# Kernel optimization log

Measured on AMD Instinct MI355X. Metric: run time of the kernel, lower is better.

Reference implementation:

```python
import jax, jax.numpy as jnp
import numpy as np

N, DIM, H, W = 8, 64, 256, 256
K = 3            # strip kernel size
EPS = 1e-5       # BatchNorm eps


def setup_inputs() -> dict:
    key = jax.random.key(0)
    kx, kh, kw = jax.random.split(key, 3)
    x = jax.random.normal(kx, (N, DIM, H, W), jnp.float32)

    def branch_params(k):
        k1, k2, k3, k4, k5 = jax.random.split(k, 5)
        w = jax.random.normal(k1, (DIM * K, DIM), jnp.float32) / np.sqrt(DIM).astype(np.float32)
        g = jax.random.uniform(k2, (DIM * K,), jnp.float32, 0.5, 1.5)   # BN weight
        b = jax.random.normal(k3, (DIM * K,), jnp.float32) * 0.1       # BN bias
        m = jax.random.normal(k4, (DIM * K,), jnp.float32) * 0.1       # BN running_mean
        v = jax.random.uniform(k5, (DIM * K,), jnp.float32, 0.5, 1.5)  # BN running_var
        return w, g, b, m, v

    wH, gH, bH, mH, vH = branch_params(kh)
    wW, gW, bW, mW, vW = branch_params(kw)
    return dict(x=x, wH=wH, gH=gH, bH=bH, mH=mH, vH=vH,
                wW=wW, gW=gW, bW=bW, mW=mW, vW=vW)


def _strip_att(x, w, g, b, m, v, horizontal):
    # Dynamic per-sample, per-channel 1D strip filter (involution-style).
    n, c, h, wd = x.shape
    gap = x.mean(axis=(2, 3))                       # (n, c)  AdaptiveAvgPool2d(1,1)
    f = gap @ w.T                                   # (n, c*K) 1x1 conv, no bias
    f = (f - m) * (g / jnp.sqrt(v + EPS)) + b       # BatchNorm2d (eval mode)
    f = jnp.tanh(f).reshape(n, c, K)                # per-(sample,channel) kernel taps
    pad = (K - 1) // 2
    if horizontal:  # kernel (1, K), reflect-pad width
        xp = jnp.pad(x, ((0, 0), (0, 0), (0, 0), (pad, pad)), mode='reflect')
        win = jnp.stack([xp[..., j:j + wd] for j in range(K)], axis=-1)  # (n,c,h,w,K)
    else:           # kernel (K, 1), reflect-pad height
        xp = jnp.pad(x, ((0, 0), (0, 0), (pad, pad), (0, 0)), mode='reflect')
        win = jnp.stack([xp[:, :, j:j + h, :] for j in range(K)], axis=-1)
    # grouped conv with groups = n*dim == depthwise correlation with dynamic taps
    return jnp.einsum('nchwk,nck->nchw', win, f)


def reference(x, wH, gH, bH, mH, vH, wW, gW, bW, mW, vW):
    out1 = _strip_att(x, wH, gH, bH, mH, vH, True)   # H_spatial_att (1,K) kernel
    out2 = _strip_att(x, wW, gW, bW, mW, vW, False)  # W_spatial_att (K,1) kernel
    return jnp.concatenate((out1, out2), axis=1)     # (n, 2c, h, w)
```

## Files before the change

kernel.cpp:

```cpp
#include <hip/hip_runtime.h>
#include <math.h>

#define N 8
#define DIM 64
#define H 256
#define W 256
#define K 3
#define EPS 1e-5f
#define TH 32

__global__ void gap_kernel(const float* __restrict__ x, float* __restrict__ gap) {
    const int plane = blockIdx.x;
    const float4* p4 = (const float4*)(x + (size_t)plane * (H * W));
    const int tid = threadIdx.x;
    float s = 0.f;
    #pragma unroll 4
    for (int i = tid; i < (H * W) / 4; i += 256) {
        float4 v = p4[i];
        s += (v.x + v.y) + (v.z + v.w);
    }
    __shared__ float red[256];
    red[tid] = s;
    __syncthreads();
    for (int off = 128; off > 0; off >>= 1) {
        if (tid < off) red[tid] += red[tid + off];
        __syncthreads();
    }
    if (tid == 0) gap[plane] = red[0] * (1.0f / (H * W));
}

__global__ void taps_kernel(const float* __restrict__ gap,
                            const float* __restrict__ wH, const float* __restrict__ gH,
                            const float* __restrict__ bH, const float* __restrict__ mH,
                            const float* __restrict__ vH,
                            const float* __restrict__ wW, const float* __restrict__ gW,
                            const float* __restrict__ bW, const float* __restrict__ mW,
                            const float* __restrict__ vW,
                            float* __restrict__ taps) {
    int idx = blockIdx.x * blockDim.x + threadIdx.x;
    if (idx >= 2 * N * DIM * K) return;
    const int branch = idx / (N * DIM * K);
    const int rem    = idx % (N * DIM * K);
    const int n      = rem / (DIM * K);
    const int j      = rem % (DIM * K);
    const float* w = branch ? wW : wH;
    const float* g = branch ? gW : gH;
    const float* b = branch ? bW : bH;
    const float* m = branch ? mW : mH;
    const float* v = branch ? vW : vH;
    const float* grow = gap + n * DIM;
    const float* wrow = w + (size_t)j * DIM;
    float acc = 0.f;
    #pragma unroll
    for (int d = 0; d < DIM; d++) acc += grow[d] * wrow[d];
    float f = (acc - m[j]) * (g[j] * rsqrtf(v[j] + EPS)) + b[j];
    taps[idx] = tanhf(f);
}

__global__ __launch_bounds__(256) void conv_kernel(const float* __restrict__ x,
                                                   const float* __restrict__ taps,
                                                   float* __restrict__ out) {
    __shared__ float tile[TH + 2][W];
    const int plane = blockIdx.y;
    const int n = plane / DIM;
    const int c = plane % DIM;
    const int h0 = blockIdx.x * TH;
    const int w = threadIdx.x;

    const float* xp = x + (size_t)plane * (H * W);

    #pragma unroll
    for (int r = 0; r < TH + 2; r++) {
        int hh = h0 - 1 + r;
        if (hh < 0) hh = -hh;
        if (hh >= H) hh = 2 * H - 2 - hh;
        tile[r][w] = xp[hh * W + w];
    }
    __syncthreads();

    const float* tH = taps + (n * DIM + c) * K;
    const float* tW = taps + N * DIM * K + (n * DIM + c) * K;
    const float tH0 = tH[0], tH1 = tH[1], tH2 = tH[2];
    const float tW0 = tW[0], tW1 = tW[1], tW2 = tW[2];

    float* out1 = out + (((size_t)n * 2 * DIM + c) * H + h0) * W;
    float* out2 = out + (((size_t)n * 2 * DIM + DIM + c) * H + h0) * W;

    const int wm = (w == 0) ? 1 : w - 1;
    const int wp = (w == W - 1) ? W - 2 : w + 1;

    #pragma unroll 4
    for (int r = 0; r < TH; r++) {
        const float xc = tile[r + 1][w];
        const float o1 = tile[r + 1][wm] * tH0 + xc * tH1 + tile[r + 1][wp] * tH2;
        const float o2 = tile[r][w] * tW0 + xc * tW1 + tile[r + 2][w] * tW2;
        out1[r * W + w] = o1;
        out2[r * W + w] = o2;
    }
}

extern "C" void kernel_launch(void* const* d_in, const int* in_sizes, int n_in,
                              void* d_out, int out_size, void* d_ws, size_t ws_size,
                              hipStream_t stream) {
    const float* x  = (const float*)d_in[0];
    const float* wH = (const float*)d_in[1];
    const float* gH = (const float*)d_in[2];
    const float* bH = (const float*)d_in[3];
    const float* mH = (const float*)d_in[4];
    const float* vH = (const float*)d_in[5];
    const float* wW = (const float*)d_in[6];
    const float* gW = (const float*)d_in[7];
    const float* bW = (const float*)d_in[8];
    const float* mW = (const float*)d_in[9];
    const float* vW = (const float*)d_in[10];
    float* out = (float*)d_out;

    float* gap  = (float*)d_ws;
    float* taps = gap + N * DIM;

    gap_kernel<<<N * DIM, 256, 0, stream>>>(x, gap);

    const int ntaps = 2 * N * DIM * K;
    taps_kernel<<<(ntaps + 255) / 256, 256, 0, stream>>>(gap, wH, gH, bH, mH, vH,
                                                         wW, gW, bW, mW, vW, taps);

    dim3 grid(H / TH, N * DIM);
    conv_kernel<<<grid, 256, 0, stream>>>(x, taps, out);
}
```

Before: 399.8 us.

## Fuse tap computation into conv kernel and vectorize tile loads and stores

Removes the separate taps kernel. Each conv block now computes its own six taps in shared memory from the pooled means, which saves one launch and a global round trip. The halo tile load and the output stores switch to float4, and each thread computes four adjacent outputs per row. The GAP reduction block grows to 512 threads. The trade-off is redundant tap work: eight blocks per plane each do six 64-element dot products.

```diff
diff --git a/kernel.cpp b/kernel.cpp
--- a/kernel.cpp
+++ b/kernel.cpp
@@ -9,93 +9,110 @@
 #define EPS 1e-5f
 #define TH 32
 
-__global__ void gap_kernel(const float* __restrict__ x, float* __restrict__ gap) {
+__global__ __launch_bounds__(512) void gap_kernel(const float* __restrict__ x,
+                                                  float* __restrict__ gap) {
     const int plane = blockIdx.x;
     const float4* p4 = (const float4*)(x + (size_t)plane * (H * W));
     const int tid = threadIdx.x;
     float s = 0.f;
     #pragma unroll 4
-    for (int i = tid; i < (H * W) / 4; i += 256) {
+    for (int i = tid; i < (H * W) / 4; i += 512) {
         float4 v = p4[i];
         s += (v.x + v.y) + (v.z + v.w);
     }
-    __shared__ float red[256];
+    __shared__ float red[512];
     red[tid] = s;
     __syncthreads();
-    for (int off = 128; off > 0; off >>= 1) {
+    for (int off = 256; off > 0; off >>= 1) {
         if (tid < off) red[tid] += red[tid + off];
         __syncthreads();
     }
     if (tid == 0) gap[plane] = red[0] * (1.0f / (H * W));
 }
 
-__global__ void taps_kernel(const float* __restrict__ gap,
-                            const float* __restrict__ wH, const float* __restrict__ gH,
-                            const float* __restrict__ bH, const float* __restrict__ mH,
-                            const float* __restrict__ vH,
-                            const float* __restrict__ wW, const float* __restrict__ gW,
-                            const float* __restrict__ bW, const float* __restrict__ mW,
-                            const float* __restrict__ vW,
-                            float* __restrict__ taps) {
-    int idx = blockIdx.x * blockDim.x + threadIdx.x;
-    if (idx >= 2 * N * DIM * K) return;
-    const int branch = idx / (N * DIM * K);
-    const int rem    = idx % (N * DIM * K);
-    const int n      = rem / (DIM * K);
-    const int j      = rem % (DIM * K);
-    const float* w = branch ? wW : wH;
-    const float* g = branch ? gW : gH;
-    const float* b = branch ? bW : bH;
-    const float* m = branch ? mW : mH;
-    const float* v = branch ? vW : vH;
-    const float* grow = gap + n * DIM;
-    const float* wrow = w + (size_t)j * DIM;
-    float acc = 0.f;
-    #pragma unroll
-    for (int d = 0; d < DIM; d++) acc += grow[d] * wrow[d];
-    float f = (acc - m[j]) * (g[j] * rsqrtf(v[j] + EPS)) + b[j];
-    taps[idx] = tanhf(f);
-}
+__global__ __launch_bounds__(256) void conv_kernel(const float* __restrict__ x,
+                                                   const float* __restrict__ gap,
+                                                   const float* __restrict__ wH,
+                                                   const float* __restrict__ gH,
+                                                   const float* __restrict__ bH,
+                                                   const float* __restrict__ mH,
+                                                   const float* __restrict__ vH,
+                                                   const float* __restrict__ wW,
+                                                   const float* __restrict__ gW,
+                                                   const float* __restrict__ bW,
+                                                   const float* __restrict__ mW,
+                                                   const float* __restrict__ vW,
+                                                   float* __restrict__ out) {
+    __shared__ float tile[(TH + 2) * W];
+    __shared__ float s_taps[6];
 
-__global__ __launch_bounds__(256) void conv_kernel(const float* __restrict__ x,
-                                                   const float* __restrict__ taps,
-                                                   float* __restrict__ out) {
-    __shared__ float tile[TH + 2][W];
     const int plane = blockIdx.y;
     const int n = plane / DIM;
     const int c = plane % DIM;
     const int h0 = blockIdx.x * TH;
-    const int w = threadIdx.x;
+    const int tid = threadIdx.x;
 
-    const float* xp = x + (size_t)plane * (H * W);
+    if (tid < 6) {
+        const int br = tid / K;
+        const int k  = tid % K;
+        const int j  = c * K + k;
+        const float* w = br ? wW : wH;
+        const float* g = br ? gW : gH;
+        const float* b = br ? bW : bH;
+        const float* m = br ? mW : mH;
+        const float* v = br ? vW : vH;
+        const float* grow = gap + n * DIM;
+        const float* wrow = w + (size_t)j * DIM;
+        float acc = 0.f;
+        #pragma unroll
+        for (int d = 0; d < DIM; d++) acc += grow[d] * wrow[d];
+        float f = (acc - m[j]) * (g[j] * rsqrtf(v[j] + EPS)) + b[j];
+        s_taps[tid] = tanhf(f);
+    }
 
-    #pragma unroll
-    for (int r = 0; r < TH + 2; r++) {
-        int hh = h0 - 1 + r;
-        if (hh < 0) hh = -hh;
-        if (hh >= H) hh = 2 * H - 2 - hh;
-        tile[r][w] = xp[hh * W + w];
+    const float4* xp4 = (const float4*)(x + (size_t)plane * (H * W));
+    float4* t4 = (float4*)tile;
+    for (int idx = tid; idx < (TH + 2) * W / 4; idx += 256) {
+        const int row = idx >> 6;
+        int hh = h0 - 1 + row;
+        if (hh < 0) hh = 1;
+        else if (hh >= H) hh = 2 * H - 2 - hh;
+        t4[idx] = xp4[hh * (W / 4) + (idx & 63)];
     }
     __syncthreads();
 
-    const float* tH = taps + (n * DIM + c) * K;
-    const float* tW = taps + N * DIM * K + (n * DIM + c) * K;
-    const float tH0 = tH[0], tH1 = tH[1], tH2 = tH[2];
-    const float tW0 = tW[0], tW1 = tW[1], tW2 = tW[2];
+    const float tH0 = s_taps[0], tH1 = s_taps[1], tH2 = s_taps[2];
+    const float tW0 = s_taps[3], tW1 = s_taps[4], tW2 = s_taps[5];
 
-    float* out1 = out + (((size_t)n * 2 * DIM + c) * H + h0) * W;
-    float* out2 = out + (((size_t)n * 2 * DIM + DIM + c) * H + h0) * W;
+    const int tx = tid & 63;
+    const int ty = tid >> 6;
 
-    const int wm = (w == 0) ? 1 : w - 1;
-    const int wp = (w == W - 1) ? W - 2 : w + 1;
+    float4* o1 = (float4*)out + ((size_t)(n * 2 * DIM + c) * H + h0) * (W / 4);
+    float4* o2 = (float4*)out + ((size_t)(n * 2 * DIM + DIM + c) * H + h0) * (W / 4);
 
-    #pragma unroll 4
-    for (int r = 0; r < TH; r++) {
-        const float xc = tile[r + 1][w];
-        const float o1 = tile[r + 1][wm] * tH0 + xc * tH1 + tile[r + 1][wp] * tH2;
-        const float o2 = tile[r][w] * tW0 + xc * tW1 + tile[r + 2][w] * tW2;
-        out1[r * W + w] = o1;
-        out2[r * W + w] = o2;
+    #pragma unroll
+    for (int r = 0; r < TH / 4; r++) {
+        const int row = r * 4 + ty;
+        const float* rc = tile + (row + 1) * W;
+        const float4 cc = ((const float4*)rc)[tx];
+        const float4 up = ((const float4*)(tile + row * W))[tx];
+        const float4 dn = ((const float4*)(tile + (row + 2) * W))[tx];
+        const float lf = (tx == 0)  ? cc.y : rc[4 * tx - 1];
+        const float rt = (tx == 63) ? cc.z : rc[4 * tx + 4];
+
+        float4 r1, r2;
+        r1.x = lf   * tH0 + cc.x * tH1 + cc.y * tH2;
+        r1.y = cc.x * tH0 + cc.y * tH1 + cc.z * tH2;
+        r1.z = cc.y * tH0 + cc.z * tH1 + cc.w * tH2;
+        r1.w = cc.z * tH0 + cc.w * tH1 + rt   * tH2;
+
+        r2.x = up.x * tW0 + cc.x * tW1 + dn.x * tW2;
+        r2.y = up.y * tW0 + cc.y * tW1 + dn.y * tW2;
+        r2.z = up.z * tW0 + cc.z * tW1 + dn.z * tW2;
+        r2.w = up.w * tW0 + cc.w * tW1 + dn.w * tW2;
+
+        o1[row * (W / 4) + tx] = r1;
+        o2[row * (W / 4) + tx] = r2;
     }
 }
 
@@ -115,15 +132,11 @@
     const float* vW = (const float*)d_in[10];
     float* out = (float*)d_out;
 
-    float* gap  = (float*)d_ws;
-    float* taps = gap + N * DIM;
+    float* gap = (float*)d_ws;
 
-    gap_kernel<<<N * DIM, 256, 0, stream>>>(x, gap);
-
-    const int ntaps = 2 * N * DIM * K;
-    taps_kernel<<<(ntaps + 255) / 256, 256, 0, stream>>>(gap, wH, gH, bH, mH, vH,
-                                                         wW, gW, bW, mW, vW, taps);
+    gap_kernel<<<N * DIM, 512, 0, stream>>>(x, gap);
 
     dim3 grid(H / TH, N * DIM);
-    conv_kernel<<<grid, 256, 0, stream>>>(x, taps, out);
+    conv_kernel<<<grid, 256, 0, stream>>>(x, gap, wH, gH, bH, mH, vH,
+                                          wW, gW, bW, mW, vW, out);
 }
```

Result: no change. 402.9 us (+0.8%).
